# Performance work log

Measured on AMD Instinct MI355X. Metric: run time of the kernel, lower is better.

Reference implementation:

```python
import jax, jax.numpy as jnp
import numpy as np

B, S, DIN, DQ, DK = 8, 2048, 1024, 64, 64

def setup_inputs() -> dict:
    key = jax.random.key(0)
    ks = jax.random.split(key, 8)
    sc = 0.02
    return {
        "input_tensor": jax.random.normal(ks[0], (B, S, DIN), jnp.float32),
        "attention_mask": jax.random.randint(ks[1], (B, 1, S), 0, 2) == 1,
        "Wq": jax.random.normal(ks[2], (DIN, DQ), jnp.float32) * sc,
        "bq": jnp.zeros((DQ,), jnp.float32),
        "Wk": jax.random.normal(ks[3], (DIN, DK), jnp.float32) * sc,
        "bk": jnp.zeros((DK,), jnp.float32),
        "Wv": jax.random.normal(ks[4], (DIN, DK), jnp.float32) * sc,
        "bv": jnp.zeros((DK,), jnp.float32),
    }

def reference(input_tensor, attention_mask, Wq, bq, Wk, bk, Wv, bv):
    q = input_tensor @ Wq + bq          # [B,S,DQ]
    k = input_tensor @ Wk + bk          # [B,S,DK]
    v = input_tensor @ Wv + bv          # [B,S,DK]
    # NOTE: original scales by sqrt(query.size(1)) == sqrt(seq_len), faithfully kept
    scale = q.shape[1] ** 0.5
    scores = jnp.einsum('bqd,bkd->bqk', q, k) / scale
    scores = jnp.where(attention_mask, jnp.float32(-1e9), scores)
    attn = jax.nn.softmax(scores, axis=-1)
    context = jnp.einsum('bqk,bkd->bqd', attn, v)
    return context
```

## Files before the change

### kernel.cpp

```cpp
#include <hip/hip_runtime.h>
#include <hip/hip_bf16.h>

#define NB 8
#define SEQ 2048
#define DIN 1024
#define DH 64

typedef __attribute__((ext_vector_type(8))) short bf16x8;
typedef __attribute__((ext_vector_type(4))) float f32x4;

static __device__ __forceinline__ unsigned short f2bf(float f) {
    unsigned int u = __builtin_bit_cast(unsigned int, f);
    unsigned int r = (u + 0x7FFFu + ((u >> 16) & 1u)) >> 16;
    return (unsigned short)r;
}

static __device__ __forceinline__ unsigned int cvt_pk_bf16(float lo, float hi) {
    unsigned int d;
    asm volatile("v_cvt_pk_bf16_f32 %0, %1, %2" : "=v"(d) : "v"(lo), "v"(hi));
    return d;
}

__global__ __launch_bounds__(256) void prep_kernel(
    const float* __restrict__ Wq, const float* __restrict__ Wk, const float* __restrict__ Wv,
    unsigned short* __restrict__ Wfrag)
{
    int j = blockIdx.x * 256 + threadIdx.x;
    int mat = j >> 16;
    int rem = j & 65535;
    int k = rem >> 6;
    int c = rem & 63;
    const float* W = (mat == 0) ? Wq : ((mat == 1) ? Wk : Wv);
    float v = W[rem];
    int col = mat * 64 + c;
    int cg = col >> 4, cl = col & 15;
    int kk = k >> 5, kq = (k >> 3) & 3, ke = k & 7;
    Wfrag[(size_t)(cg * 32 + kk) * 512 + cl * 32 + kq * 8 + ke] = f2bf(v);
}

__global__ __launch_bounds__(256, 2) void qkv_kernel(
    const float* __restrict__ X, const unsigned short* __restrict__ Wfrag,
    const float* __restrict__ bq, const float* __restrict__ bk, const float* __restrict__ bv,
    unsigned short* __restrict__ Qb, unsigned short* __restrict__ Kb, unsigned short* __restrict__ Vt)
{
    __shared__ __align__(16) short As[2][32][128];

    const int tid = threadIdx.x;
    const int w   = tid >> 6;
    const int l   = tid & 63;
    const int l15 = l & 15;
    const int lq  = l >> 4;
    const int row0 = blockIdx.x * 32;

    f32x4 acc[2][3] = {};

    const float* xb = X + (size_t)row0 * DIN;

    const unsigned short* wfb[3];
    #pragma unroll
    for (int n = 0; n < 3; ++n)
        wfb[n] = Wfrag + (size_t)((w * 3 + n) * 32) * 512 + (l15 * 4 + lq) * 8;

    float4 pf[2][4];
    #pragma unroll
    for (int i = 0; i < 4; ++i) {
        int c = tid + 256 * i;
        const float* p = xb + (size_t)(c >> 5) * DIN + (c & 31) * 4;
        pf[0][i] = *(const float4*)(p);
        pf[1][i] = *(const float4*)(p + 128);
    }

    bf16x8 wb[3][3];
    #pragma unroll
    for (int n = 0; n < 3; ++n) wb[0][n] = *(const bf16x8*)(wfb[n]);
    #pragma unroll
    for (int n = 0; n < 3; ++n) wb[1][n] = *(const bf16x8*)(wfb[n] + 512);

    #pragma unroll
    for (int step = 0; step < 8; ++step) {
        const int pi = step & 1;

        unsigned int u[8];
        #pragma unroll
        for (int i = 0; i < 4; ++i) {
            u[2 * i]     = cvt_pk_bf16(pf[pi][i].x, pf[pi][i].y);
            u[2 * i + 1] = cvt_pk_bf16(pf[pi][i].z, pf[pi][i].w);
        }
        #pragma unroll
        for (int i = 0; i < 4; ++i) {
            int c = tid + 256 * i;
            int r = c >> 5;
            int bo = ((c & 31) * 8) ^ ((r & 7) << 4);
            uint2 v2; v2.x = u[2 * i]; v2.y = u[2 * i + 1];
            *(uint2*)((char*)&As[pi][r][0] + bo) = v2;
        }
        if (step + 2 < 8) {
            #pragma unroll
            for (int i = 0; i < 4; ++i) {
                int c = tid + 256 * i;
                pf[pi][i] = *(const float4*)(xb + (size_t)(c >> 5) * DIN + (step + 2) * 128 + (c & 31) * 4);
            }
        }
        __syncthreads();

        #pragma unroll
        for (int kkl = 0; kkl < 4; ++kkl) {
            const int c = step * 4 + kkl;
            if (c + 2 < 32) {
                #pragma unroll
                for (int n = 0; n < 3; ++n)
                    wb[(c + 2) % 3][n] = *(const bf16x8*)(wfb[n] + (size_t)(c + 2) * 512);
            }
            bf16x8 a[2];
            #pragma unroll
            for (int m = 0; m < 2; ++m) {
                int r = m * 16 + l15;
                int bo = ((kkl * 32 + lq * 8) * 2) ^ ((r & 7) << 4);
                a[m] = *(const bf16x8*)((const char*)&As[pi][r][0] + bo);
            }
            #pragma unroll
            for (int m = 0; m < 2; ++m)
                #pragma unroll
                for (int n = 0; n < 3; ++n)
                    acc[m][n] = __builtin_amdgcn_mfma_f32_16x16x32_bf16(a[m], wb[c % 3][n], acc[m][n], 0, 0, 0);
        }
    }

    #pragma unroll
    for (int n = 0; n < 3; ++n) {
        int col = w * 48 + n * 16 + l15;
        int mat = col >> 6, c = col & 63;
        float badd = ((mat == 0) ? bq : ((mat == 1) ? bk : bv))[c];
        #pragma unroll
        for (int m = 0; m < 2; ++m) {
            #pragma unroll
            for (int reg = 0; reg < 4; ++reg) {
                int row = row0 + m * 16 + lq * 4 + reg;
                unsigned short v16 = f2bf(acc[m][n][reg] + badd);
                if (mat == 0)      Qb[(size_t)row * DH + c] = v16;
                else if (mat == 1) Kb[(size_t)row * DH + c] = v16;
                else {
                    int bb = row >> 11, ss = row & 2047;
                    Vt[((size_t)(bb * DH + c)) * SEQ + ss] = v16;
                }
            }
        }
    }
}

#define KT 128
#define NT (SEQ / KT)
#define PPITCH 36

__global__ __launch_bounds__(512, 4) void attn_kernel(
    const unsigned short* __restrict__ Qb, const unsigned short* __restrict__ Kb,
    const unsigned short* __restrict__ Vt, const int* __restrict__ mask,
    float* __restrict__ out)
{
    __shared__ __align__(16) unsigned char smem[32768 + 8 * 32 * PPITCH * 2 + 8 * 32 * 4];
    short (*Ks)[DH]         = reinterpret_cast<short (*)[DH]>(smem);
    short (*Vs)[KT]         = reinterpret_cast<short (*)[KT]>(smem + 16384);
    short (*ps)[32][PPITCH] = reinterpret_cast<short (*)[32][PPITCH]>(smem + 32768);
    float (*sml)[32]        = reinterpret_cast<float (*)[32]>(smem + 32768 + 8 * 32 * PPITCH * 2);
    float (*Om)[68]         = reinterpret_cast<float (*)[68]>(smem);

    const int tid = threadIdx.x;
    const int w   = tid >> 6;
    const int l   = tid & 63;
    const int l15 = l & 15;
    const int lq  = l >> 4;
    const int wqh = w >> 2;
    const int wkq = w & 3;

    int bid = blockIdx.x;
    bid = (bid & 7) * 32 + (bid >> 3);
    const int b  = bid >> 5;
    const int q0 = (bid & 31) * 64;

    bf16x8 aq[2][2];
    #pragma unroll
    for (int m = 0; m < 2; ++m)
        #pragma unroll
        for (int kk = 0; kk < 2; ++kk)
            aq[m][kk] = *(const bf16x8*)(Qb + ((size_t)(b * SEQ + q0 + wqh * 32 + m * 16 + l15)) * DH + kk * 32 + lq * 8);

    const int krow = tid >> 3;
    const int kcol = (tid & 7) * 8;
    const int kdst = kcol ^ ((krow & 7) << 3);
    const int vrow = tid >> 4;
    const int vcol = (tid & 15) * 8;
    const int vdst = vcol ^ ((vrow & 7) << 3);

    const unsigned short* Kbase = Kb + (size_t)(b * SEQ) * DH + kcol;
    const unsigned short* Vbase = Vt + (size_t)(b * DH) * SEQ + vcol;

    bf16x8 kr[2], vr[2];
    #pragma unroll
    for (int i = 0; i < 2; ++i) {
        kr[i] = *(const bf16x8*)(Kbase + (size_t)(i * 64 + krow) * DH);
        vr[i] = *(const bf16x8*)(Vbase + (size_t)(i * 32 + vrow) * SEQ);
    }

    f32x4 o[2][4];
    #pragma unroll
    for (int m = 0; m < 2; ++m)
        #pragma unroll
        for (int n = 0; n < 4; ++n) o[m][n] = f32x4{0, 0, 0, 0};
    float lr[2][4] = {};

    const float rscale = 0.022097086912079612f;
    const int kw = wkq * 32;
    const int* mbase = mask + b * SEQ + kw + l15;

    for (int t = 0; t < NT; ++t) {
        #pragma unroll
        for (int i = 0; i < 2; ++i) *(bf16x8*)&Ks[i * 64 + krow][kdst] = kr[i];
        #pragma unroll
        for (int i = 0; i < 2; ++i) *(bf16x8*)&Vs[i * 32 + vrow][vdst] = vr[i];

        int mk0 = mbase[t * KT];
        int mk1 = mbase[t * KT + 16];

        if (t + 1 < NT) {
            const int key0n = (t + 1) * KT;
            #pragma unroll
            for (int i = 0; i < 2; ++i) {
                kr[i] = *(const bf16x8*)(Kbase + (size_t)(key0n + i * 64 + krow) * DH);
                vr[i] = *(const bf16x8*)(Vbase + (size_t)(i * 32 + vrow) * SEQ + key0n);
            }
        }

        __syncthreads();

        bf16x8 bkf[2][2];
        #pragma unroll
        for (int n = 0; n < 2; ++n)
            #pragma unroll
            for (int kk = 0; kk < 2; ++kk)
                bkf[n][kk] = *(const bf16x8*)&Ks[kw + n * 16 + l15][(kk * 32 + lq * 8) ^ ((l15 & 7) << 3)];
        f32x4 s[2][2];
        #pragma unroll
        for (int m = 0; m < 2; ++m)
            #pragma unroll
            for (int n = 0; n < 2; ++n) s[m][n] = f32x4{0, 0, 0, 0};
        #pragma unroll
        for (int kk = 0; kk < 2; ++kk)
            #pragma unroll
            for (int m = 0; m < 2; ++m)
                #pragma unroll
                for (int n = 0; n < 2; ++n)
                    s[m][n] = __builtin_amdgcn_mfma_f32_16x16x32_bf16(aq[m][kk], bkf[n][kk], s[m][n], 0, 0, 0);

        float bb0 = mk0 ? -1e30f : 0.0f;
        float bb1 = mk1 ? -1e30f : 0.0f;
        #pragma unroll
        for (int m = 0; m < 2; ++m)
            #pragma unroll
            for (int n = 0; n < 2; ++n) {
                float bvv = n ? bb1 : bb0;
                #pragma unroll
                for (int r = 0; r < 4; ++r) {
                    float p = __expf(fmaf(s[m][n][r], rscale, bvv));
                    lr[m][r] += p;
                    ps[w][m * 16 + lq * 4 + r][n * 16 + l15] = (short)f2bf(p);
                }
            }

        bf16x8 pa[2];
        #pragma unroll
        for (int m = 0; m < 2; ++m)
            pa[m] = *(const bf16x8*)&ps[w][m * 16 + l15][lq * 8];
        bf16x8 bvf[4];
        #pragma unroll
        for (int n = 0; n < 4; ++n)
            bvf[n] = *(const bf16x8*)&Vs[n * 16 + l15][(kw + lq * 8) ^ ((l15 & 7) << 3)];
        #pragma unroll
        for (int m = 0; m < 2; ++m)
            #pragma unroll
            for (int n = 0; n < 4; ++n)
                o[m][n] = __builtin_amdgcn_mfma_f32_16x16x32_bf16(pa[m], bvf[n], o[m][n], 0, 0, 0);

        __syncthreads();
    }

    #pragma unroll
    for (int off = 1; off < 16; off <<= 1)
        #pragma unroll
        for (int m = 0; m < 2; ++m)
            #pragma unroll
            for (int r = 0; r < 4; ++r) lr[m][r] += __shfl_xor(lr[m][r], off);
    if (l15 == 0) {
        #pragma unroll
        for (int m = 0; m < 2; ++m)
            #pragma unroll
            for (int r = 0; r < 4; ++r) sml[w][m * 16 + lq * 4 + r] = lr[m][r];
    }

    #pragma unroll
    for (int rnd = 0; rnd < 4; ++rnd) {
        __syncthreads();
        if (wkq == rnd) {
            #pragma unroll
            for (int m = 0; m < 2; ++m)
                #pragma unroll
                for (int n = 0; n < 4; ++n)
                    #pragma unroll
                    for (int r = 0; r < 4; ++r) {
                        int row = wqh * 32 + m * 16 + lq * 4 + r;
                        int col = n * 16 + l15;
                        if (rnd == 0) Om[row][col] = o[m][n][r];
                        else          Om[row][col] += o[m][n][r];
                    }
        }
    }
    __syncthreads();

    {
        int q  = tid >> 3;
        int d0 = (tid & 7) * 8;
        int wb = (q >> 5) * 4;
        float lt = sml[wb][q & 31] + sml[wb + 1][q & 31] + sml[wb + 2][q & 31] + sml[wb + 3][q & 31];
        float inv = 1.0f / lt;
        float vx[8];
        #pragma unroll
        for (int j = 0; j < 8; ++j) vx[j] = Om[q][d0 + j] * inv;
        float* op = out + ((size_t)(b * SEQ + q0 + q)) * DH + d0;
        float4 r0; r0.x = vx[0]; r0.y = vx[1]; r0.z = vx[2]; r0.w = vx[3];
        float4 r1; r1.x = vx[4]; r1.y = vx[5]; r1.z = vx[6]; r1.w = vx[7];
        *(float4*)op = r0;
        *(float4*)(op + 4) = r1;
    }
}

extern "C" void kernel_launch(void* const* d_in, const int* in_sizes, int n_in,
                              void* d_out, int out_size, void* d_ws, size_t ws_size,
                              hipStream_t stream) {
    const float* X    = (const float*)d_in[0];
    const int*   mask = (const int*)d_in[1];
    const float* Wq   = (const float*)d_in[2];
    const float* bq   = (const float*)d_in[3];
    const float* Wk   = (const float*)d_in[4];
    const float* bk   = (const float*)d_in[5];
    const float* Wv   = (const float*)d_in[6];
    const float* bv   = (const float*)d_in[7];
    float* out = (float*)d_out;

    char* ws = (char*)d_ws;
    unsigned short* Qb = (unsigned short*)(ws);
    unsigned short* Kb = (unsigned short*)(ws + (2u << 20));
    unsigned short* Vt = (unsigned short*)(ws + (4u << 20));
    unsigned short* Wfrag = (unsigned short*)(ws + (6u << 20));

    prep_kernel<<<768, 256, 0, stream>>>(Wq, Wk, Wv, Wfrag);
    qkv_kernel<<<512, 256, 0, stream>>>(X, Wfrag, bq, bk, bv, Qb, Kb, Vt);
    attn_kernel<<<256, 512, 0, stream>>>(Qb, Kb, Vt, mask, out);
}
```

Baseline: 60.47 us.

## Split attention over key ranges with partial outputs and a merge kernel

The attention kernel now splits each query tile's keys into four 512-key chunks across separate 256-thread blocks, producing 1024 blocks instead of 256. Each block writes unnormalized partial outputs and row sums to workspace, and a new merge kernel sums them and normalizes. K/V shared tiles are double-buffered, which drops the per-iteration trailing barrier. The QKV kernel also deepens its weight-fragment register prefetch from 3 to 6 stages. This trades extra global traffic and a kernel launch for more parallelism and less synchronization.

```diff
diff --git a/kernel.cpp b/kernel.cpp
--- a/kernel.cpp
+++ b/kernel.cpp
@@ -47,9 +47,8 @@
 
     const int tid = threadIdx.x;
     const int w   = tid >> 6;
-    const int l   = tid & 63;
-    const int l15 = l & 15;
-    const int lq  = l >> 4;
+    const int l15 = tid & 15;
+    const int lq  = (tid >> 4) & 3;
     const int row0 = blockIdx.x * 32;
 
     f32x4 acc[2][3] = {};
@@ -70,11 +69,12 @@
         pf[1][i] = *(const float4*)(p + 128);
     }
 
-    bf16x8 wb[3][3];
-    #pragma unroll
-    for (int n = 0; n < 3; ++n) wb[0][n] = *(const bf16x8*)(wfb[n]);
-    #pragma unroll
-    for (int n = 0; n < 3; ++n) wb[1][n] = *(const bf16x8*)(wfb[n] + 512);
+    bf16x8 wb[6][3];
+    #pragma unroll
+    for (int s = 0; s < 6; ++s)
+        #pragma unroll
+        for (int n = 0; n < 3; ++n)
+            wb[s][n] = *(const bf16x8*)(wfb[n] + (size_t)s * 512);
 
     #pragma unroll
     for (int step = 0; step < 8; ++step) {
@@ -106,11 +106,6 @@
         #pragma unroll
         for (int kkl = 0; kkl < 4; ++kkl) {
             const int c = step * 4 + kkl;
-            if (c + 2 < 32) {
-                #pragma unroll
-                for (int n = 0; n < 3; ++n)
-                    wb[(c + 2) % 3][n] = *(const bf16x8*)(wfb[n] + (size_t)(c + 2) * 512);
-            }
             bf16x8 a[2];
             #pragma unroll
             for (int m = 0; m < 2; ++m) {
@@ -122,7 +117,12 @@
             for (int m = 0; m < 2; ++m)
                 #pragma unroll
                 for (int n = 0; n < 3; ++n)
-                    acc[m][n] = __builtin_amdgcn_mfma_f32_16x16x32_bf16(a[m], wb[c % 3][n], acc[m][n], 0, 0, 0);
+                    acc[m][n] = __builtin_amdgcn_mfma_f32_16x16x32_bf16(a[m], wb[c % 6][n], acc[m][n], 0, 0, 0);
+            if (c + 6 < 32) {
+                #pragma unroll
+                for (int n = 0; n < 3; ++n)
+                    wb[c % 6][n] = *(const bf16x8*)(wfb[n] + (size_t)(c + 6) * 512);
+            }
         }
     }
 
@@ -148,57 +148,54 @@
     }
 }
 
-#define KT 128
-#define NT (SEQ / KT)
-#define PPITCH 36
-
-__global__ __launch_bounds__(512, 4) void attn_kernel(
+#define AKT 64
+#define ANT 8
+#define PP 36
+
+__global__ __launch_bounds__(256, 3) void attn_kernel(
     const unsigned short* __restrict__ Qb, const unsigned short* __restrict__ Kb,
     const unsigned short* __restrict__ Vt, const int* __restrict__ mask,
-    float* __restrict__ out)
+    float* __restrict__ Opart, float* __restrict__ lpart)
 {
-    __shared__ __align__(16) unsigned char smem[32768 + 8 * 32 * PPITCH * 2 + 8 * 32 * 4];
-    short (*Ks)[DH]         = reinterpret_cast<short (*)[DH]>(smem);
-    short (*Vs)[KT]         = reinterpret_cast<short (*)[KT]>(smem + 16384);
-    short (*ps)[32][PPITCH] = reinterpret_cast<short (*)[32][PPITCH]>(smem + 32768);
-    float (*sml)[32]        = reinterpret_cast<float (*)[32]>(smem + 32768 + 8 * 32 * PPITCH * 2);
-    float (*Om)[68]         = reinterpret_cast<float (*)[68]>(smem);
+    __shared__ __align__(16) short Ks[2][AKT][DH];
+    __shared__ __align__(16) short Vs[2][DH][AKT];
+    __shared__ __align__(16) short ps[4][32][PP];
+    __shared__ float sml[4][32];
 
     const int tid = threadIdx.x;
     const int w   = tid >> 6;
-    const int l   = tid & 63;
-    const int l15 = l & 15;
-    const int lq  = l >> 4;
-    const int wqh = w >> 2;
-    const int wkq = w & 3;
+    const int l15 = tid & 15;
+    const int lq  = (tid >> 4) & 3;
+    const int wm  = w >> 1;
+    const int wn  = w & 1;
 
     int bid = blockIdx.x;
-    bid = (bid & 7) * 32 + (bid >> 3);
-    const int b  = bid >> 5;
-    const int q0 = (bid & 31) * 64;
+    int sbid = (bid & 7) * 128 + (bid >> 3);
+    const int b   = sbid >> 7;
+    const int qt  = (sbid >> 2) & 31;
+    const int kq  = sbid & 3;
+    const int q0  = qt * 64;
+    const int kb0 = kq * 512;
 
     bf16x8 aq[2][2];
     #pragma unroll
     for (int m = 0; m < 2; ++m)
         #pragma unroll
         for (int kk = 0; kk < 2; ++kk)
-            aq[m][kk] = *(const bf16x8*)(Qb + ((size_t)(b * SEQ + q0 + wqh * 32 + m * 16 + l15)) * DH + kk * 32 + lq * 8);
-
-    const int krow = tid >> 3;
-    const int kcol = (tid & 7) * 8;
-    const int kdst = kcol ^ ((krow & 7) << 3);
-    const int vrow = tid >> 4;
-    const int vcol = (tid & 15) * 8;
-    const int vdst = vcol ^ ((vrow & 7) << 3);
-
-    const unsigned short* Kbase = Kb + (size_t)(b * SEQ) * DH + kcol;
-    const unsigned short* Vbase = Vt + (size_t)(b * DH) * SEQ + vcol;
+            aq[m][kk] = *(const bf16x8*)(Qb + ((size_t)(b * SEQ + q0 + wm * 32 + m * 16 + l15)) * DH + kk * 32 + lq * 8);
+
+    const int srow = tid >> 3;
+    const int scol = (tid & 7) * 8;
+    const int sdst = scol ^ ((srow & 7) << 3);
+
+    const unsigned short* Kst = Kb + ((size_t)(b * SEQ) + kb0 + srow) * DH + scol;
+    const unsigned short* Vst = Vt + ((size_t)(b * DH) + srow) * SEQ + kb0 + scol;
 
     bf16x8 kr[2], vr[2];
     #pragma unroll
     for (int i = 0; i < 2; ++i) {
-        kr[i] = *(const bf16x8*)(Kbase + (size_t)(i * 64 + krow) * DH);
-        vr[i] = *(const bf16x8*)(Vbase + (size_t)(i * 32 + vrow) * SEQ);
+        kr[i] = *(const bf16x8*)(Kst + (size_t)(i * 32) * DH);
+        vr[i] = *(const bf16x8*)(Vst + (size_t)(i * 32) * SEQ);
     }
 
     f32x4 o[2][4];
@@ -209,24 +206,24 @@
     float lr[2][4] = {};
 
     const float rscale = 0.022097086912079612f;
-    const int kw = wkq * 32;
-    const int* mbase = mask + b * SEQ + kw + l15;
-
-    for (int t = 0; t < NT; ++t) {
-        #pragma unroll
-        for (int i = 0; i < 2; ++i) *(bf16x8*)&Ks[i * 64 + krow][kdst] = kr[i];
-        #pragma unroll
-        for (int i = 0; i < 2; ++i) *(bf16x8*)&Vs[i * 32 + vrow][vdst] = vr[i];
-
-        int mk0 = mbase[t * KT];
-        int mk1 = mbase[t * KT + 16];
-
-        if (t + 1 < NT) {
-            const int key0n = (t + 1) * KT;
+    const int* mbase = mask + b * SEQ + kb0 + wn * 32 + l15;
+
+    for (int t = 0; t < ANT; ++t) {
+        const int cur = t & 1;
+
+        #pragma unroll
+        for (int i = 0; i < 2; ++i) *(bf16x8*)&Ks[cur][i * 32 + srow][sdst] = kr[i];
+        #pragma unroll
+        for (int i = 0; i < 2; ++i) *(bf16x8*)&Vs[cur][i * 32 + srow][sdst] = vr[i];
+
+        int mk0 = mbase[t * AKT];
+        int mk1 = mbase[t * AKT + 16];
+
+        if (t + 1 < ANT) {
             #pragma unroll
             for (int i = 0; i < 2; ++i) {
-                kr[i] = *(const bf16x8*)(Kbase + (size_t)(key0n + i * 64 + krow) * DH);
-                vr[i] = *(const bf16x8*)(Vbase + (size_t)(i * 32 + vrow) * SEQ + key0n);
+                kr[i] = *(const bf16x8*)(Kst + (size_t)((t + 1) * AKT + i * 32) * DH);
+                vr[i] = *(const bf16x8*)(Vst + (size_t)(i * 32) * SEQ + (t + 1) * AKT);
             }
         }
 
@@ -236,8 +233,10 @@
         #pragma unroll
         for (int n = 0; n < 2; ++n)
             #pragma unroll
-            for (int kk = 0; kk < 2; ++kk)
-                bkf[n][kk] = *(const bf16x8*)&Ks[kw + n * 16 + l15][(kk * 32 + lq * 8) ^ ((l15 & 7) << 3)];
+            for (int kk = 0; kk < 2; ++kk) {
+                int row = wn * 32 + n * 16 + l15;
+                bkf[n][kk] = *(const bf16x8*)&Ks[cur][row][(kk * 32 + lq * 8) ^ ((row & 7) << 3)];
+            }
         f32x4 s[2][2];
         #pragma unroll
         for (int m = 0; m < 2; ++m)
@@ -272,15 +271,15 @@
             pa[m] = *(const bf16x8*)&ps[w][m * 16 + l15][lq * 8];
         bf16x8 bvf[4];
         #pragma unroll
-        for (int n = 0; n < 4; ++n)
-            bvf[n] = *(const bf16x8*)&Vs[n * 16 + l15][(kw + lq * 8) ^ ((l15 & 7) << 3)];
+        for (int n = 0; n < 4; ++n) {
+            int row = n * 16 + l15;
+            bvf[n] = *(const bf16x8*)&Vs[cur][row][(wn * 32 + lq * 8) ^ ((row & 7) << 3)];
+        }
         #pragma unroll
         for (int m = 0; m < 2; ++m)
             #pragma unroll
             for (int n = 0; n < 4; ++n)
                 o[m][n] = __builtin_amdgcn_mfma_f32_16x16x32_bf16(pa[m], bvf[n], o[m][n], 0, 0, 0);
-
-        __syncthreads();
     }
 
     #pragma unroll
@@ -295,40 +294,71 @@
             #pragma unroll
             for (int r = 0; r < 4; ++r) sml[w][m * 16 + lq * 4 + r] = lr[m][r];
     }
-
-    #pragma unroll
-    for (int rnd = 0; rnd < 4; ++rnd) {
-        __syncthreads();
-        if (wkq == rnd) {
-            #pragma unroll
-            for (int m = 0; m < 2; ++m)
-                #pragma unroll
-                for (int n = 0; n < 4; ++n)
-                    #pragma unroll
-                    for (int r = 0; r < 4; ++r) {
-                        int row = wqh * 32 + m * 16 + lq * 4 + r;
-                        int col = n * 16 + l15;
-                        if (rnd == 0) Om[row][col] = o[m][n][r];
-                        else          Om[row][col] += o[m][n][r];
-                    }
-        }
-    }
     __syncthreads();
 
+    float (*mg)[32][64] = reinterpret_cast<float (*)[32][64]>(&Ks[0][0][0]);
+    if (wn == 1) {
+        #pragma unroll
+        for (int m = 0; m < 2; ++m)
+            #pragma unroll
+            for (int n = 0; n < 4; ++n)
+                #pragma unroll
+                for (int r = 0; r < 4; ++r)
+                    mg[wm][m * 16 + lq * 4 + r][n * 16 + l15] = o[m][n][r];
+    }
+    __syncthreads();
+    if (wn == 0) {
+        #pragma unroll
+        for (int m = 0; m < 2; ++m)
+            #pragma unroll
+            for (int n = 0; n < 4; ++n)
+                #pragma unroll
+                for (int r = 0; r < 4; ++r)
+                    mg[wm][m * 16 + lq * 4 + r][n * 16 + l15] += o[m][n][r];
+    }
+    __syncthreads();
+
     {
-        int q  = tid >> 3;
-        int d0 = (tid & 7) * 8;
-        int wb = (q >> 5) * 4;
-        float lt = sml[wb][q & 31] + sml[wb + 1][q & 31] + sml[wb + 2][q & 31] + sml[wb + 3][q & 31];
-        float inv = 1.0f / lt;
-        float vx[8];
-        #pragma unroll
-        for (int j = 0; j < 8; ++j) vx[j] = Om[q][d0 + j] * inv;
-        float* op = out + ((size_t)(b * SEQ + q0 + q)) * DH + d0;
-        float4 r0; r0.x = vx[0]; r0.y = vx[1]; r0.z = vx[2]; r0.w = vx[3];
-        float4 r1; r1.x = vx[4]; r1.y = vx[5]; r1.z = vx[6]; r1.w = vx[7];
-        *(float4*)op = r0;
-        *(float4*)(op + 4) = r1;
+        int qq = tid >> 2;
+        int d0 = (tid & 3) * 16;
+        float* dst = Opart + ((size_t)kq * (NB * SEQ) + b * SEQ + q0 + qq) * DH + d0;
+        #pragma unroll
+        for (int j = 0; j < 4; ++j)
+            *(float4*)(dst + j * 4) = *(float4*)&mg[qq >> 5][qq & 31][d0 + j * 4];
+    }
+    if (tid < 64) {
+        int wmi = tid >> 5;
+        float lsum = sml[wmi * 2][tid & 31] + sml[wmi * 2 + 1][tid & 31];
+        lpart[(size_t)kq * (NB * SEQ) + b * SEQ + q0 + tid] = lsum;
+    }
+}
+
+__global__ __launch_bounds__(256) void merge_kernel(
+    const float* __restrict__ Opart, const float* __restrict__ lpart,
+    float* __restrict__ out)
+{
+    int bid = blockIdx.x;
+    int sbid = (bid & 7) * 32 + (bid >> 3);
+    int g = sbid * 256 + threadIdx.x;
+    int q  = g >> 2;
+    int d0 = (g & 3) * 16;
+
+    float l = lpart[q] + lpart[16384 + q] + lpart[2 * 16384 + q] + lpart[3 * 16384 + q];
+    float inv = 1.0f / l;
+
+    const float* o0 = Opart + (size_t)q * DH + d0;
+    #pragma unroll
+    for (int j = 0; j < 4; ++j) {
+        float4 a = *(const float4*)(o0 + j * 4);
+        float4 b2 = *(const float4*)(o0 + (size_t)16384 * DH + j * 4);
+        float4 c = *(const float4*)(o0 + (size_t)2 * 16384 * DH + j * 4);
+        float4 d = *(const float4*)(o0 + (size_t)3 * 16384 * DH + j * 4);
+        float4 r;
+        r.x = (a.x + b2.x + c.x + d.x) * inv;
+        r.y = (a.y + b2.y + c.y + d.y) * inv;
+        r.z = (a.z + b2.z + c.z + d.z) * inv;
+        r.w = (a.w + b2.w + c.w + d.w) * inv;
+        *(float4*)(out + (size_t)q * DH + d0 + j * 4) = r;
     }
 }
 
@@ -346,12 +376,15 @@
     float* out = (float*)d_out;
 
     char* ws = (char*)d_ws;
-    unsigned short* Qb = (unsigned short*)(ws);
-    unsigned short* Kb = (unsigned short*)(ws + (2u << 20));
-    unsigned short* Vt = (unsigned short*)(ws + (4u << 20));
+    unsigned short* Qb    = (unsigned short*)(ws);
+    unsigned short* Kb    = (unsigned short*)(ws + (2u << 20));
+    unsigned short* Vt    = (unsigned short*)(ws + (4u << 20));
     unsigned short* Wfrag = (unsigned short*)(ws + (6u << 20));
+    float* Opart          = (float*)(ws + (8u << 20));
+    float* lpart          = (float*)(ws + (24u << 20));
 
     prep_kernel<<<768, 256, 0, stream>>>(Wq, Wk, Wv, Wfrag);
     qkv_kernel<<<512, 256, 0, stream>>>(X, Wfrag, bq, bk, bv, Qb, Kb, Vt);
-    attn_kernel<<<256, 512, 0, stream>>>(Qb, Kb, Vt, mask, out);
-}
+    attn_kernel<<<1024, 256, 0, stream>>>(Qb, Kb, Vt, mask, Opart, lpart);
+    merge_kernel<<<256, 256, 0, stream>>>(Opart, lpart, out);
+}
```

Result: no change. 61.08 us (+1.0%).
